# Optimization experiments

Measured on AMD Instinct MI355X. Metric: run time of the kernel, lower is better.

## Reference

```python
import jax, jax.numpy as jnp
import numpy as np
from jax import lax

NPOINT, RADIUS, NSAMPLE = 512, 0.2, 32
MLP, IN_CH = (64, 64, 128), 6
BN_EPS = 1e-5


def square_distance(src, dst):
    # src [B,S,3], dst [B,N,3] -> [B,S,N]
    d = -2.0 * jnp.einsum('bsc,bnc->bsn', src, dst)
    d += jnp.sum(src ** 2, -1)[:, :, None]
    d += jnp.sum(dst ** 2, -1)[:, None, :]
    return d


def farthest_point_sample(xyz, npoint):
    # deterministic start at index 0 (torch version uses randint)
    B, N, _ = xyz.shape
    init_dist = jnp.full((B, N), 1e10, dtype=xyz.dtype)
    init_far = jnp.zeros((B,), dtype=jnp.int32)

    def step(carry, _):
        distance, farthest = carry
        centroid = jnp.take_along_axis(xyz, farthest[:, None, None], axis=1)  # [B,1,3]
        dist = jnp.sum((xyz - centroid) ** 2, -1)  # [B,N]
        distance = jnp.minimum(distance, dist)
        nxt = jnp.argmax(distance, -1).astype(jnp.int32)
        return (distance, nxt), farthest

    _, cents = lax.scan(step, (init_dist, init_far), None, length=npoint)
    return cents.T  # [B, npoint]


def index_points(points, idx):
    # points [B,N,C], idx [B,...] -> [B,...,C]
    return jax.vmap(lambda p, i: p[i])(points, idx)


def query_ball_point(radius, nsample, xyz, new_xyz):
    B, N, _ = xyz.shape
    sqr = square_distance(new_xyz, xyz)  # [B,S,N]
    gi = jnp.where(sqr > radius ** 2, N, jnp.arange(N, dtype=jnp.int32)[None, None, :])
    gi = jnp.sort(gi, axis=-1)[:, :, :nsample]  # [B,S,K]
    first = gi[:, :, :1]
    return jnp.where(gi == N, first, gi)


def setup_inputs():
    key = jax.random.key(0)
    ks = jax.random.split(key, 2 + len(MLP))
    B, N = 16, 4096
    inp = {
        'xyz': jax.random.normal(ks[0], (B, N, 3), dtype=jnp.float32),
        'points': jax.random.normal(ks[1], (B, N, 3), dtype=jnp.float32),
    }
    last = IN_CH
    for i, oc in enumerate(MLP):
        inp[f'w{i}'] = jax.random.normal(ks[2 + i], (oc, last), dtype=jnp.float32) / np.sqrt(last)
        inp[f'b{i}'] = jnp.zeros((oc,), dtype=jnp.float32)
        inp[f'gamma{i}'] = jnp.ones((oc,), dtype=jnp.float32)
        inp[f'beta{i}'] = jnp.zeros((oc,), dtype=jnp.float32)
        last = oc
    return inp


def reference(xyz, points, w0, b0, gamma0, beta0, w1, b1, gamma1, beta1, w2, b2, gamma2, beta2):
    B, N, C = xyz.shape
    S = NPOINT
    fps_idx = lax.stop_gradient(farthest_point_sample(xyz, NPOINT))  # [B,S]
    new_xyz = index_points(xyz, fps_idx)  # [B,S,3]
    idx = lax.stop_gradient(query_ball_point(RADIUS, NSAMPLE, xyz, new_xyz))  # [B,S,K]
    grouped_xyz = index_points(xyz, idx)  # [B,S,K,3]
    grouped_xyz_norm = grouped_xyz - new_xyz[:, :, None, :]
    grouped_points = index_points(points, idx)  # [B,S,K,D]
    feats = jnp.concatenate([grouped_xyz_norm, grouped_points], axis=-1)  # [B,S,K,3+D]

    # shared MLP: 1x1 conv + BatchNorm (batch stats, train-mode) + ReLU, channel-last
    params = [(w0, b0, gamma0, beta0), (w1, b1, gamma1, beta1), (w2, b2, gamma2, beta2)]
    for w, b, g, be in params:
        feats = jnp.einsum('bskc,oc->bsko', feats, w) + b
        mean = jnp.mean(feats, axis=(0, 1, 2))
        var = jnp.var(feats, axis=(0, 1, 2))
        feats = (feats - mean) * lax.rsqrt(var + BN_EPS) * g + be
        feats = jax.nn.relu(feats)

    new_points = jnp.max(feats, axis=2)  # max over nsample -> [B,S,C_out]
    return new_xyz, new_points
```

## Files before the change

### kernel.cpp

```cpp
#include <hip/hip_runtime.h>

#define NPT    4096
#define NBATCH 16
#define NS     512
#define KSAMP  32
#define MROWS  (NBATCH*NS*KSAMP)
#define RC2    0.04f
#define NZSTAT 3288

using bf16x8 = __attribute__((ext_vector_type(8))) short;
using f32x4  = __attribute__((ext_vector_type(4))) float;
using f32x2  = __attribute__((ext_vector_type(2))) float;
#define MFMA16(A,B,C) __builtin_amdgcn_mfma_f32_16x16x32_bf16(A,B,C,0,0,0)

__device__ __forceinline__ unsigned short f2bf(float f) {
  unsigned u = __float_as_uint(f);
  unsigned r = (u + 0x7FFFu + ((u >> 16) & 1u)) >> 16;
  return (unsigned short)r;
}
__device__ __forceinline__ float bf2f(unsigned short h) {
  return __uint_as_float(((unsigned)h) << 16);
}
__device__ __forceinline__ void atomAddF64(double* p, double v) {
  unsafeAtomicAdd(p, v);
}

template<int CTRL>
__device__ __forceinline__ double dpp_max(double v) {
  long long x = __double_as_longlong(v);
  int lo = __builtin_amdgcn_update_dpp(0, (int)(x & 0xFFFFFFFFll), CTRL, 0xf, 0xf, true);
  int hi = __builtin_amdgcn_update_dpp(0, (int)(x >> 32),          CTRL, 0xf, 0xf, true);
  return fmax(v, __hiloint2double(hi, lo));
}

__global__ __launch_bounds__(512) void fps_wconv_kernel(const float* __restrict__ xyz,
                                                        float* __restrict__ out_newxyz,
                                                        float* __restrict__ ws_newxyz,
                                                        const float* __restrict__ w0,
                                                        const float* __restrict__ w1,
                                                        const float* __restrict__ w2,
                                                        unsigned short* __restrict__ wbf0,
                                                        unsigned short* __restrict__ wbf1,
                                                        unsigned short* __restrict__ wbf2,
                                                        double* __restrict__ statz)
{
  const int t = threadIdx.x;
  const int b = blockIdx.x;
  if (b == NBATCH) {
    if (t < 64) {
#pragma unroll
      for (int c = 0; c < 8; ++c)
        wbf0[t*8 + c] = (c < 6) ? f2bf(w0[t*6 + c]) : (unsigned short)0;
    }
    for (int i = t; i < 64*64; i += 512) wbf1[i] = f2bf(w1[i]);
    for (int i = t; i < 128*64; i += 512) wbf2[i] = f2bf(w2[i]);
    for (int i = t; i < NZSTAT; i += 512) statz[i] = 0.0;
    return;
  }

  __shared__ float pts[NPT*3];
  __shared__ float cent[NS*3];
  __shared__ double red[8];
  __shared__ int farslot;
  const float* xb = xyz + (size_t)b * NPT * 3;

  { const float4* s4 = (const float4*)xb;
    float4* d4 = (float4*)pts;
    for (int i = t; i < NPT*3/4; i += 512) d4[i] = s4[i]; }
  __syncthreads();

  f32x2 px[4], py[4], pz[4], dist[4];
  unsigned int loc0[4], loc1[4];
#pragma unroll
  for (int j = 0; j < 4; ++j) {
    int i0 = t + (2*j)   * 512;
    int i1 = t + (2*j+1) * 512;
    px[j] = f32x2{pts[i0*3+0], pts[i1*3+0]};
    py[j] = f32x2{pts[i0*3+1], pts[i1*3+1]};
    pz[j] = f32x2{pts[i0*3+2], pts[i1*3+2]};
    dist[j] = f32x2{1e10f, 1e10f};
    loc0[j] = ~(unsigned)i0;
    loc1[j] = ~(unsigned)i1;
  }

  const int lane = t & 63, w = t >> 6;
  int far = 0;
  for (int s = 0; s < NS; ++s) {
    const float cx = pts[far*3+0], cy = pts[far*3+1], cz = pts[far*3+2];
    if (t == 0) { cent[s*3+0] = cx; cent[s*3+1] = cy; cent[s*3+2] = cz; }
    if (s == NS-1) break;

    double best = 0.0;
    {
#pragma clang fp contract(off)
      const f32x2 vcx = {cx, cx}, vcy = {cy, cy}, vcz = {cz, cz};
#pragma unroll
      for (int j = 0; j < 4; ++j) {
        f32x2 dx = px[j] - vcx;
        f32x2 dy = py[j] - vcy;
        f32x2 dz = pz[j] - vcz;
        f32x2 dd = dx*dx + dy*dy + dz*dz;
        f32x2 nd;
        nd.x = fminf(dist[j].x, dd.x);
        nd.y = fminf(dist[j].y, dd.y);
        dist[j] = nd;
        unsigned long long k0 = ((unsigned long long)__float_as_uint(nd.x) << 32)
                              | (unsigned long long)loc0[j];
        unsigned long long k1 = ((unsigned long long)__float_as_uint(nd.y) << 32)
                              | (unsigned long long)loc1[j];
        best = fmax(best, __longlong_as_double((long long)k0));
        best = fmax(best, __longlong_as_double((long long)k1));
      }
    }
    best = dpp_max<0x111>(best);
    best = dpp_max<0x112>(best);
    best = dpp_max<0x114>(best);
    best = dpp_max<0x118>(best);
    best = dpp_max<0x142>(best);
    best = dpp_max<0x143>(best);

    if (lane == 63) red[w] = best;
    __syncthreads();
    if (w == 0) {
      double v = red[lane & 7];
      v = dpp_max<0x111>(v);
      v = dpp_max<0x112>(v);
      v = dpp_max<0x114>(v);
      if (lane == 7)
        farslot = (int)(~(unsigned)(unsigned long long)__double_as_longlong(v));
    }
    __syncthreads();
    far = farslot;
  }
  __syncthreads();
  for (int i = t; i < NS*3; i += 512) {
    float v = cent[i];
    out_newxyz[(size_t)b*NS*3 + i] = v;
    ws_newxyz[(size_t)b*NS*3 + i]  = v;
  }
}

__global__ __launch_bounds__(256) void ball_kernel(const float* __restrict__ xyz,
                                                   const float* __restrict__ pointsf,
                                                   const float* __restrict__ ws_newxyz,
                                                   unsigned short* __restrict__ featsbf,
                                                   double* __restrict__ momb)
{
  __shared__ int sel[4][KSAMP];
  __shared__ float momw[4][27];
  const int t = threadIdx.x, lane = t & 63, w = t >> 6;
  const int q = blockIdx.x * 4 + w;
  const int b = q >> 9;
  const float* xb = xyz     + (size_t)b * NPT * 3;
  const float* pb = pointsf + (size_t)b * NPT * 3;

  const float qx = ws_newxyz[q*3+0], qy = ws_newxyz[q*3+1], qz = ws_newxyz[q*3+2];
  const float q2 = __fadd_rn(__fadd_rn(__fmul_rn(qx,qx), __fmul_rn(qy,qy)), __fmul_rn(qz,qz));

  int count = 0;
  for (int c = 0; c < 64 && count < KSAMP; ++c) {
    int i = (c << 6) + lane;
    float fx = xb[i*3+0], fy = xb[i*3+1], fz = xb[i*3+2];
    float p2 = __fadd_rn(__fadd_rn(__fmul_rn(fx,fx), __fmul_rn(fy,fy)), __fmul_rn(fz,fz));
    float e  = __fadd_rn(__fadd_rn(__fmul_rn(qx,fx), __fmul_rn(qy,fy)), __fmul_rn(qz,fz));
    float d  = __fadd_rn(__fadd_rn(__fmul_rn(-2.0f, e), q2), p2);
    bool keep = (d <= RC2);
    unsigned long long mask = __ballot(keep ? 1 : 0);
    int slot = count + (int)__popcll(mask & ((1ull << lane) - 1ull));
    if (keep && slot < KSAMP) sel[w][slot] = i;
    count += (int)__popcll(mask);
  }
  __syncthreads();

  float f[6];
  const int n = (count < KSAMP) ? count : KSAMP;
  if (lane < KSAMP) {
    int id = (lane < n) ? sel[w][lane] : sel[w][0];
    float gx = xb[id*3+0], gy = xb[id*3+1], gz = xb[id*3+2];
    unsigned short hb[8];
    hb[0] = f2bf(__fsub_rn(gx, qx));
    hb[1] = f2bf(__fsub_rn(gy, qy));
    hb[2] = f2bf(__fsub_rn(gz, qz));
    hb[3] = f2bf(pb[id*3+0]);
    hb[4] = f2bf(pb[id*3+1]);
    hb[5] = f2bf(pb[id*3+2]);
    hb[6] = 0; hb[7] = 0;
    uint4 pk;
    pk.x = (unsigned)hb[0] | ((unsigned)hb[1] << 16);
    pk.y = (unsigned)hb[2] | ((unsigned)hb[3] << 16);
    pk.z = (unsigned)hb[4] | ((unsigned)hb[5] << 16);
    pk.w = 0;
    ((uint4*)featsbf)[(size_t)q * KSAMP + lane] = pk;
#pragma unroll
    for (int c2 = 0; c2 < 6; ++c2) f[c2] = bf2f(hb[c2]);
  } else {
    f[0]=f[1]=f[2]=f[3]=f[4]=f[5]=0.f;
  }

  float p[27];
#pragma unroll
  for (int c = 0; c < 6; ++c) p[c] = f[c];
  { int m = 6;
#pragma unroll
    for (int c = 0; c < 6; ++c)
#pragma unroll
      for (int d = c; d < 6; ++d) p[m++] = f[c]*f[d]; }
#pragma unroll
  for (int mm = 0; mm < 27; ++mm) {
    float v = p[mm];
#pragma unroll
    for (int off = 1; off < 64; off <<= 1) v += __shfl_xor(v, off);
    p[mm] = v;
  }
  if (lane == 0) {
#pragma unroll
    for (int mm = 0; mm < 27; ++mm) momw[w][mm] = p[mm];
  }
  __syncthreads();
  if (t < 27)
    atomAddF64(&momb[(blockIdx.x & 7)*27 + t],
               (double)(momw[0][t] + momw[1][t] + momw[2][t] + momw[3][t]));
}

template<int PASS>
__global__ __launch_bounds__(256) void mlp_kernel(
    const unsigned short* __restrict__ featsbf,
    const unsigned short* __restrict__ wbf0,
    const unsigned short* __restrict__ wbf1,
    const unsigned short* __restrict__ wbf2,
    const double* __restrict__ momb,
    const float* __restrict__ g0, const float* __restrict__ be0,
    const float* __restrict__ g1, const float* __restrict__ be1,
    const float* __restrict__ g2, const float* __restrict__ be2,
    double* __restrict__ s1g, double* __restrict__ q1g,
    double* __restrict__ s2g, double* __restrict__ q2g,
    float* __restrict__ outp)
{
  __shared__ __align__(16) unsigned short xb[256*72];
  __shared__ __align__(16) unsigned short wb[128*72];
  constexpr int SN = (PASS==1) ? 4*64 : (PASS==2 ? 4*128 : 1);
  __shared__ float ssum[SN], sqsum[SN];
  __shared__ float ssc0[64], ssh0[64], ssc1[64], ssh1[64], ssc2[128], ssh2[128];
  __shared__ double mom[27];

  unsigned short* wb0 = wb + 64*72;
  unsigned short* xf  = wb + 72*72;

  const int t = threadIdx.x, blk = blockIdx.x;
  const int lane = t & 63, w = t >> 6;
  const int lr = lane & 15, lk = lane >> 4;

  ((uint4*)xf)[t] = ((const uint4*)featsbf)[(size_t)blk*256 + t];
  if (t < 64) ((uint4*)wb0)[t] = ((const uint4*)wbf0)[t];
  { int row = t >> 2, seg = t & 3;
    const uint4* src = (const uint4*)(wbf1 + row*64 + seg*16);
    uint4* dst = (uint4*)(wb + row*72 + seg*16);
    dst[0] = src[0]; dst[1] = src[1]; }
  if (t < 27) {
    double s = 0.0;
#pragma unroll
    for (int bkt = 0; bkt < 8; ++bkt) s += momb[bkt*27 + t];
    mom[t] = s / (double)MROWS;
  }
  __syncthreads();

  if (t < 64) {
    double wv[6];
#pragma unroll
    for (int c = 0; c < 6; ++c) wv[c] = (double)bf2f(wbf0[t*8 + c]);
    double macc = 0.0;
#pragma unroll
    for (int c = 0; c < 6; ++c) macc += wv[c] * mom[c];
    double e2 = 0.0;
    int mi = 6;
#pragma unroll
    for (int c = 0; c < 6; ++c)
#pragma unroll
      for (int d = c; d < 6; ++d) {
        double coef = (c == d) ? wv[c]*wv[c] : 2.0*wv[c]*wv[d];
        e2 += coef * mom[mi++];
      }
    double var = e2 - macc*macc;
    float sc = g0[t] / sqrtf((float)var + 1e-5f);
    ssc0[t] = sc;
    ssh0[t] = be0[t] - (float)macc * sc;
  }
  if (PASS >= 2 && t < 64) {
    double s = 0.0, qq = 0.0;
#pragma unroll
    for (int bkt = 0; bkt < 8; ++bkt) { s += s1g[bkt*64 + t]; qq += q1g[bkt*64 + t]; }
    double mean = s / (double)MROWS;
    double var  = qq / (double)MROWS - mean*mean;
    float sc = g1[t] / sqrtf((float)var + 1e-5f);
    ssc1[t] = sc;
    ssh1[t] = be1[t] - (float)mean * sc;
  }
  if (PASS == 3 && t < 128) {
    double s = 0.0, qq = 0.0;
#pragma unroll
    for (int bkt = 0; bkt < 8; ++bkt) { s += s2g[bkt*128 + t]; qq += q2g[bkt*128 + t]; }
    double mean = s / (double)MROWS;
    double var  = qq / (double)MROWS - mean*mean;
    float sc = g2[t] / sqrtf((float)var + 1e-5f);
    ssc2[t] = sc;
    ssh2[t] = be2[t] - (float)mean * sc;
  }
  __syncthreads();

  const bf16x8 zb = {0,0,0,0,0,0,0,0};
  const f32x4 fz = {0.f,0.f,0.f,0.f};

  f32x4 acc[16];
#pragma unroll
  for (int i = 0; i < 16; ++i) acc[i] = fz;
  {
    bf16x8 af[4], bw[4];
#pragma unroll
    for (int i = 0; i < 4; ++i) { af[i] = zb; bw[i] = zb; }
    if (lk == 0) {
#pragma unroll
      for (int rt = 0; rt < 4; ++rt) af[rt] = *(const bf16x8*)&xf[(w*64 + rt*16 + lr)*8];
#pragma unroll
      for (int ct = 0; ct < 4; ++ct) bw[ct] = *(const bf16x8*)&wb0[(ct*16 + lr)*8];
    }
#pragma unroll
    for (int rt = 0; rt < 4; ++rt)
#pragma unroll
      for (int ct = 0; ct < 4; ++ct) acc[rt*4+ct] = MFMA16(af[rt], bw[ct], acc[rt*4+ct]);
  }
#pragma unroll
  for (int rt = 0; rt < 4; ++rt)
#pragma unroll
    for (int ct = 0; ct < 4; ++ct) {
      const int ch = ct*16 + lr;
      const float sc = ssc0[ch], sh = ssh0[ch];
#pragma unroll
      for (int r = 0; r < 4; ++r) {
        const int row = w*64 + rt*16 + lk*4 + r;
        float v = fmaxf(fmaf(acc[rt*4+ct][r], sc, sh), 0.f);
        xb[row*72 + ch] = f2bf(v);
      }
    }
  __syncthreads();

  f32x4 acc1[16];
#pragma unroll
  for (int i = 0; i < 16; ++i) acc1[i] = fz;
#pragma unroll
  for (int k0 = 0; k0 < 64; k0 += 32) {
    bf16x8 af[4], bw[4];
#pragma unroll
    for (int rt = 0; rt < 4; ++rt) af[rt] = *(const bf16x8*)&xb[(w*64 + rt*16 + lr)*72 + k0 + lk*8];
#pragma unroll
    for (int ct = 0; ct < 4; ++ct) bw[ct] = *(const bf16x8*)&wb[(ct*16 + lr)*72 + k0 + lk*8];
#pragma unroll
    for (int rt = 0; rt < 4; ++rt)
#pragma unroll
      for (int ct = 0; ct < 4; ++ct) acc1[rt*4+ct] = MFMA16(af[rt], bw[ct], acc1[rt*4+ct]);
  }

  if (PASS == 1) {
#pragma unroll
    for (int ct = 0; ct < 4; ++ct) {
      float s = 0.f, q = 0.f;
#pragma unroll
      for (int rt = 0; rt < 4; ++rt)
#pragma unroll
        for (int r = 0; r < 4; ++r) { float v = acc1[rt*4+ct][r]; s += v; q = fmaf(v, v, q); }
      s += __shfl_xor(s, 16); s += __shfl_xor(s, 32);
      q += __shfl_xor(q, 16); q += __shfl_xor(q, 32);
      if (lk == 0) { ssum[w*64 + ct*16 + lr] = s; sqsum[w*64 + ct*16 + lr] = q; }
    }
    __syncthreads();
    if (t < 64) {
      float s = ssum[t] + ssum[64+t] + ssum[128+t] + ssum[192+t];
      float q = sqsum[t] + sqsum[64+t] + sqsum[128+t] + sqsum[192+t];
      const int bkt = blk & 7;
      atomAddF64(&s1g[bkt*64 + t], (double)s);
      atomAddF64(&q1g[bkt*64 + t], (double)q);
    }
    return;
  }

  __syncthreads();

  { int row = t >> 1, seg = t & 1;
    const uint4* src = (const uint4*)(wbf2 + row*64 + seg*32);
    uint4* dst = (uint4*)(wb + row*72 + seg*32);
    dst[0] = src[0]; dst[1] = src[1]; dst[2] = src[2]; dst[3] = src[3]; }
#pragma unroll
  for (int rt = 0; rt < 4; ++rt)
#pragma unroll
    for (int ct = 0; ct < 4; ++ct) {
      const int ch = ct*16 + lr;
      const float sc = ssc1[ch], sh = ssh1[ch];
#pragma unroll
      for (int r = 0; r < 4; ++r) {
        const int row = w*64 + rt*16 + lk*4 + r;
        float v = fmaxf(fmaf(acc1[rt*4+ct][r], sc, sh), 0.f);
        xb[row*72 + ch] = f2bf(v);
      }
    }
  __syncthreads();

#pragma unroll
  for (int half = 0; half < 2; ++half) {
    f32x4 acc2[16];
#pragma unroll
    for (int i = 0; i < 16; ++i) acc2[i] = fz;
#pragma unroll
    for (int k0 = 0; k0 < 64; k0 += 32) {
      bf16x8 af[4], bw[4];
#pragma unroll
      for (int rt = 0; rt < 4; ++rt) af[rt] = *(const bf16x8*)&xb[(w*64 + rt*16 + lr)*72 + k0 + lk*8];
#pragma unroll
      for (int ct = 0; ct < 4; ++ct) bw[ct] = *(const bf16x8*)&wb[((half*4+ct)*16 + lr)*72 + k0 + lk*8];
#pragma unroll
      for (int rt = 0; rt < 4; ++rt)
#pragma unroll
        for (int ct = 0; ct < 4; ++ct) acc2[rt*4+ct] = MFMA16(af[rt], bw[ct], acc2[rt*4+ct]);
    }
    if (PASS == 2) {
#pragma unroll
      for (int ct = 0; ct < 4; ++ct) {
        float s = 0.f, q = 0.f;
#pragma unroll
        for (int rt = 0; rt < 4; ++rt)
#pragma unroll
          for (int r = 0; r < 4; ++r) { float v = acc2[rt*4+ct][r]; s += v; q = fmaf(v, v, q); }
        s += __shfl_xor(s, 16); s += __shfl_xor(s, 32);
        q += __shfl_xor(q, 16); q += __shfl_xor(q, 32);
        const int ch = (half*4+ct)*16 + lr;
        if (lk == 0) { ssum[w*128 + ch] = s; sqsum[w*128 + ch] = q; }
      }
    } else {
#pragma unroll
      for (int ct = 0; ct < 4; ++ct) {
        const int ch = (half*4+ct)*16 + lr;
        const float sc = ssc2[ch], sh = ssh2[ch];
        float ma = 0.f, mb = 0.f;
#pragma unroll
        for (int r = 0; r < 4; ++r) {
          ma = fmaxf(ma, fmaf(acc2[0*4+ct][r], sc, sh));
          ma = fmaxf(ma, fmaf(acc2[1*4+ct][r], sc, sh));
          mb = fmaxf(mb, fmaf(acc2[2*4+ct][r], sc, sh));
          mb = fmaxf(mb, fmaf(acc2[3*4+ct][r], sc, sh));
        }
        ma = fmaxf(ma, __shfl_xor(ma, 16)); ma = fmaxf(ma, __shfl_xor(ma, 32));
        mb = fmaxf(mb, __shfl_xor(mb, 16)); mb = fmaxf(mb, __shfl_xor(mb, 32));
        if (lk == 0) {
          const int q0 = blk*8 + w*2;
          outp[(size_t)q0*128 + ch]     = ma;
          outp[(size_t)(q0+1)*128 + ch] = mb;
        }
      }
    }
  }
  if (PASS == 2) {
    __syncthreads();
    if (t < 128) {
      float s = ssum[t] + ssum[128+t] + ssum[256+t] + ssum[384+t];
      float q = sqsum[t] + sqsum[128+t] + sqsum[256+t] + sqsum[384+t];
      const int bkt = blk & 7;
      atomAddF64(&s2g[bkt*128 + t], (double)s);
      atomAddF64(&q2g[bkt*128 + t], (double)q);
    }
  }
}

extern "C" void kernel_launch(void* const* d_in, const int* in_sizes, int n_in,
                              void* d_out, int out_size, void* d_ws, size_t ws_size,
                              hipStream_t stream)
{
  const float* xyz     = (const float*)d_in[0];
  const float* pointsf = (const float*)d_in[1];
  const float* w0  = (const float*)d_in[2];
  const float* g0  = (const float*)d_in[4];
  const float* be0 = (const float*)d_in[5];
  const float* w1  = (const float*)d_in[6];
  const float* g1  = (const float*)d_in[8];
  const float* be1 = (const float*)d_in[9];
  const float* w2  = (const float*)d_in[10];
  const float* g2  = (const float*)d_in[12];
  const float* be2 = (const float*)d_in[13];

  float* out        = (float*)d_out;
  float* out_newxyz = out;
  float* out_newpts = out + 24576;

  float* ws = (float*)d_ws;
  float* ws_newxyz = ws;
  unsigned short* featsbf = (unsigned short*)(ws + 24576);
  double* momb = (double*)(ws + 1073152);
  double* s1g  = momb + 216;
  double* q1g  = s1g + 512;
  double* s2g  = q1g + 512;
  double* q2g  = s2g + 1024;
  unsigned short* wbf0 = (unsigned short*)(ws + 1079728);
  unsigned short* wbf1 = (unsigned short*)(ws + 1079984);
  unsigned short* wbf2 = (unsigned short*)(ws + 1082032);

  fps_wconv_kernel<<<NBATCH + 1, 512, 0, stream>>>(xyz, out_newxyz, ws_newxyz,
      w0, w1, w2, wbf0, wbf1, wbf2, momb);
  ball_kernel<<<2048, 256, 0, stream>>>(xyz, pointsf, ws_newxyz, featsbf, momb);
  mlp_kernel<1><<<1024, 256, 0, stream>>>(featsbf, wbf0, wbf1, wbf2, momb,
      g0, be0, g1, be1, g2, be2, s1g, q1g, s2g, q2g, nullptr);
  mlp_kernel<2><<<1024, 256, 0, stream>>>(featsbf, wbf0, wbf1, wbf2, momb,
      g0, be0, g1, be1, g2, be2, s1g, q1g, s2g, q2g, nullptr);
  mlp_kernel<3><<<1024, 256, 0, stream>>>(featsbf, wbf0, wbf1, wbf2, momb,
      g0, be0, g1, be1, g2, be2, s1g, q1g, s2g, q2g, out_newpts);
}
```

Measured before the change: 446.9 us.

## Fuse ball query and three MLP passes into one cooperative kernel with grid syncs

Merges the ball-query kernel and the three MLP stat/output passes into a single cooperative mega-kernel of 512 persistent blocks, separated by grid-wide syncs. Each block loops over several tiles and computes BN scale/shift only once per pass. This is meant to remove the launch gaps and tail effects between four kernels. The FPS reduction also drops its second block barrier by double-buffering the per-wave maxima so every thread reduces them directly. Risks: grid.sync cost, lower occupancy from the combined shared memory, and a fallback to the old multi-kernel path if the cooperative launch fails.

```diff
diff --git a/kernel.cpp b/kernel.cpp
--- a/kernel.cpp
+++ b/kernel.cpp
@@ -1,4 +1,6 @@
 #include <hip/hip_runtime.h>
+#include <hip/hip_cooperative_groups.h>
+namespace cg = cooperative_groups;
 
 #define NPT    4096
 #define NBATCH 16
@@ -60,8 +62,7 @@
 
   __shared__ float pts[NPT*3];
   __shared__ float cent[NS*3];
-  __shared__ double red[8];
-  __shared__ int farslot;
+  __shared__ __align__(16) double red[2][8];
   const float* xb = xyz + (size_t)b * NPT * 3;
 
   { const float4* s4 = (const float4*)xb;
@@ -119,18 +120,14 @@
     best = dpp_max<0x142>(best);
     best = dpp_max<0x143>(best);
 
-    if (lane == 63) red[w] = best;
+    if (lane == 63) red[s & 1][w] = best;
     __syncthreads();
-    if (w == 0) {
-      double v = red[lane & 7];
-      v = dpp_max<0x111>(v);
-      v = dpp_max<0x112>(v);
-      v = dpp_max<0x114>(v);
-      if (lane == 7)
-        farslot = (int)(~(unsigned)(unsigned long long)__double_as_longlong(v));
-    }
-    __syncthreads();
-    far = farslot;
+    { const double2* r2 = (const double2*)red[s & 1];
+      double2 a = r2[0], b2 = r2[1], c = r2[2], d = r2[3];
+      double m = fmax(fmax(fmax(a.x, a.y), fmax(b2.x, b2.y)),
+                      fmax(fmax(c.x, c.y), fmax(d.x, d.y)));
+      far = (int)(~(unsigned)(unsigned long long)__double_as_longlong(m));
+    }
   }
   __syncthreads();
   for (int i = t; i < NS*3; i += 512) {
@@ -140,16 +137,27 @@
   }
 }
 
-__global__ __launch_bounds__(256) void ball_kernel(const float* __restrict__ xyz,
-                                                   const float* __restrict__ pointsf,
-                                                   const float* __restrict__ ws_newxyz,
-                                                   unsigned short* __restrict__ featsbf,
-                                                   double* __restrict__ momb)
-{
-  __shared__ int sel[4][KSAMP];
-  __shared__ float momw[4][27];
+struct __align__(16) MlpSmem {
+  unsigned short xb[256*72];
+  unsigned short wb[128*72];
+  float ssum[512], sqsum[512];
+  float ssc0[64], ssh0[64], ssc1[64], ssh1[64], ssc2[128], ssh2[128];
+  double mom[27];
+};
+struct BallSmem {
+  int sel[4][KSAMP];
+  float momw[4][27];
+};
+
+__device__ __forceinline__ void ball_tile(int tile, BallSmem& bs,
+                                          const float* __restrict__ xyz,
+                                          const float* __restrict__ pointsf,
+                                          const float* __restrict__ ws_newxyz,
+                                          unsigned short* __restrict__ featsbf,
+                                          double* __restrict__ momb)
+{
   const int t = threadIdx.x, lane = t & 63, w = t >> 6;
-  const int q = blockIdx.x * 4 + w;
+  const int q = tile * 4 + w;
   const int b = q >> 9;
   const float* xb = xyz     + (size_t)b * NPT * 3;
   const float* pb = pointsf + (size_t)b * NPT * 3;
@@ -167,7 +175,7 @@
     bool keep = (d <= RC2);
     unsigned long long mask = __ballot(keep ? 1 : 0);
     int slot = count + (int)__popcll(mask & ((1ull << lane) - 1ull));
-    if (keep && slot < KSAMP) sel[w][slot] = i;
+    if (keep && slot < KSAMP) bs.sel[w][slot] = i;
     count += (int)__popcll(mask);
   }
   __syncthreads();
@@ -175,7 +183,7 @@
   float f[6];
   const int n = (count < KSAMP) ? count : KSAMP;
   if (lane < KSAMP) {
-    int id = (lane < n) ? sel[w][lane] : sel[w][0];
+    int id = (lane < n) ? bs.sel[w][lane] : bs.sel[w][0];
     float gx = xb[id*3+0], gy = xb[id*3+1], gz = xb[id*3+2];
     unsigned short hb[8];
     hb[0] = f2bf(__fsub_rn(gx, qx));
@@ -184,7 +192,6 @@
     hb[3] = f2bf(pb[id*3+0]);
     hb[4] = f2bf(pb[id*3+1]);
     hb[5] = f2bf(pb[id*3+2]);
-    hb[6] = 0; hb[7] = 0;
     uint4 pk;
     pk.x = (unsigned)hb[0] | ((unsigned)hb[1] << 16);
     pk.y = (unsigned)hb[2] | ((unsigned)hb[3] << 16);
@@ -214,12 +221,304 @@
   }
   if (lane == 0) {
 #pragma unroll
-    for (int mm = 0; mm < 27; ++mm) momw[w][mm] = p[mm];
+    for (int mm = 0; mm < 27; ++mm) bs.momw[w][mm] = p[mm];
   }
   __syncthreads();
   if (t < 27)
-    atomAddF64(&momb[(blockIdx.x & 7)*27 + t],
-               (double)(momw[0][t] + momw[1][t] + momw[2][t] + momw[3][t]));
+    atomAddF64(&momb[(tile & 7)*27 + t],
+               (double)(bs.momw[0][t] + bs.momw[1][t] + bs.momw[2][t] + bs.momw[3][t]));
+  __syncthreads();
+}
+
+template<int PASS>
+__device__ __forceinline__ void mlp_tile(int tile, int prolog, MlpSmem& sm,
+    const unsigned short* __restrict__ featsbf,
+    const unsigned short* __restrict__ wbf0,
+    const unsigned short* __restrict__ wbf1,
+    const unsigned short* __restrict__ wbf2,
+    const double* __restrict__ momb,
+    const float* __restrict__ g0, const float* __restrict__ be0,
+    const float* __restrict__ g1, const float* __restrict__ be1,
+    const float* __restrict__ g2, const float* __restrict__ be2,
+    double* __restrict__ s1g, double* __restrict__ q1g,
+    double* __restrict__ s2g, double* __restrict__ q2g,
+    float* __restrict__ outp)
+{
+  unsigned short* wb0 = sm.wb + 64*72;
+  unsigned short* xf  = sm.wb + 72*72;
+
+  const int t = threadIdx.x;
+  const int lane = t & 63, w = t >> 6;
+  const int lr = lane & 15, lk = lane >> 4;
+
+  ((uint4*)xf)[t] = ((const uint4*)featsbf)[(size_t)tile*256 + t];
+  if (t < 64) ((uint4*)wb0)[t] = ((const uint4*)wbf0)[t];
+  { int row = t >> 2, seg = t & 3;
+    const uint4* src = (const uint4*)(wbf1 + row*64 + seg*16);
+    uint4* dst = (uint4*)(sm.wb + row*72 + seg*16);
+    dst[0] = src[0]; dst[1] = src[1]; }
+  if ((prolog & 1) && t < 27) {
+    double s = 0.0;
+#pragma unroll
+    for (int bkt = 0; bkt < 8; ++bkt) s += momb[bkt*27 + t];
+    sm.mom[t] = s / (double)MROWS;
+  }
+  __syncthreads();
+
+  if ((prolog & 1) && t < 64) {
+    double wv[6];
+#pragma unroll
+    for (int c = 0; c < 6; ++c) wv[c] = (double)bf2f(wbf0[t*8 + c]);
+    double macc = 0.0;
+#pragma unroll
+    for (int c = 0; c < 6; ++c) macc += wv[c] * sm.mom[c];
+    double e2 = 0.0;
+    int mi = 6;
+#pragma unroll
+    for (int c = 0; c < 6; ++c)
+#pragma unroll
+      for (int d = c; d < 6; ++d) {
+        double coef = (c == d) ? wv[c]*wv[c] : 2.0*wv[c]*wv[d];
+        e2 += coef * sm.mom[mi++];
+      }
+    double var = e2 - macc*macc;
+    float sc = g0[t] / sqrtf((float)var + 1e-5f);
+    sm.ssc0[t] = sc;
+    sm.ssh0[t] = be0[t] - (float)macc * sc;
+  }
+  if ((prolog & 2) && t < 64) {
+    double s = 0.0, qq = 0.0;
+#pragma unroll
+    for (int bkt = 0; bkt < 8; ++bkt) { s += s1g[bkt*64 + t]; qq += q1g[bkt*64 + t]; }
+    double mean = s / (double)MROWS;
+    double var  = qq / (double)MROWS - mean*mean;
+    float sc = g1[t] / sqrtf((float)var + 1e-5f);
+    sm.ssc1[t] = sc;
+    sm.ssh1[t] = be1[t] - (float)mean * sc;
+  }
+  if ((prolog & 4) && t < 128) {
+    double s = 0.0, qq = 0.0;
+#pragma unroll
+    for (int bkt = 0; bkt < 8; ++bkt) { s += s2g[bkt*128 + t]; qq += q2g[bkt*128 + t]; }
+    double mean = s / (double)MROWS;
+    double var  = qq / (double)MROWS - mean*mean;
+    float sc = g2[t] / sqrtf((float)var + 1e-5f);
+    sm.ssc2[t] = sc;
+    sm.ssh2[t] = be2[t] - (float)mean * sc;
+  }
+  __syncthreads();
+
+  const bf16x8 zb = {0,0,0,0,0,0,0,0};
+  const f32x4 fz = {0.f,0.f,0.f,0.f};
+
+  f32x4 acc[16];
+#pragma unroll
+  for (int i = 0; i < 16; ++i) acc[i] = fz;
+  {
+    bf16x8 af[4], bw[4];
+#pragma unroll
+    for (int i = 0; i < 4; ++i) { af[i] = zb; bw[i] = zb; }
+    if (lk == 0) {
+#pragma unroll
+      for (int rt = 0; rt < 4; ++rt) af[rt] = *(const bf16x8*)&xf[(w*64 + rt*16 + lr)*8];
+#pragma unroll
+      for (int ct = 0; ct < 4; ++ct) bw[ct] = *(const bf16x8*)&wb0[(ct*16 + lr)*8];
+    }
+#pragma unroll
+    for (int rt = 0; rt < 4; ++rt)
+#pragma unroll
+      for (int ct = 0; ct < 4; ++ct) acc[rt*4+ct] = MFMA16(af[rt], bw[ct], acc[rt*4+ct]);
+  }
+#pragma unroll
+  for (int rt = 0; rt < 4; ++rt)
+#pragma unroll
+    for (int ct = 0; ct < 4; ++ct) {
+      const int ch = ct*16 + lr;
+      const float sc = sm.ssc0[ch], sh = sm.ssh0[ch];
+#pragma unroll
+      for (int r = 0; r < 4; ++r) {
+        const int row = w*64 + rt*16 + lk*4 + r;
+        float v = fmaxf(fmaf(acc[rt*4+ct][r], sc, sh), 0.f);
+        sm.xb[row*72 + ch] = f2bf(v);
+      }
+    }
+  __syncthreads();
+
+  f32x4 acc1[16];
+#pragma unroll
+  for (int i = 0; i < 16; ++i) acc1[i] = fz;
+#pragma unroll
+  for (int k0 = 0; k0 < 64; k0 += 32) {
+    bf16x8 af[4], bw[4];
+#pragma unroll
+    for (int rt = 0; rt < 4; ++rt) af[rt] = *(const bf16x8*)&sm.xb[(w*64 + rt*16 + lr)*72 + k0 + lk*8];
+#pragma unroll
+    for (int ct = 0; ct < 4; ++ct) bw[ct] = *(const bf16x8*)&sm.wb[(ct*16 + lr)*72 + k0 + lk*8];
+#pragma unroll
+    for (int rt = 0; rt < 4; ++rt)
+#pragma unroll
+      for (int ct = 0; ct < 4; ++ct) acc1[rt*4+ct] = MFMA16(af[rt], bw[ct], acc1[rt*4+ct]);
+  }
+
+  if constexpr (PASS == 1) {
+#pragma unroll
+    for (int ct = 0; ct < 4; ++ct) {
+      float s = 0.f, q = 0.f;
+#pragma unroll
+      for (int rt = 0; rt < 4; ++rt)
+#pragma unroll
+        for (int r = 0; r < 4; ++r) { float v = acc1[rt*4+ct][r]; s += v; q = fmaf(v, v, q); }
+      s += __shfl_xor(s, 16); s += __shfl_xor(s, 32);
+      q += __shfl_xor(q, 16); q += __shfl_xor(q, 32);
+      if (lk == 0) { sm.ssum[w*64 + ct*16 + lr] = s; sm.sqsum[w*64 + ct*16 + lr] = q; }
+    }
+    __syncthreads();
+    if (t < 64) {
+      float s = sm.ssum[t] + sm.ssum[64+t] + sm.ssum[128+t] + sm.ssum[192+t];
+      float q = sm.sqsum[t] + sm.sqsum[64+t] + sm.sqsum[128+t] + sm.sqsum[192+t];
+      const int bkt = tile & 7;
+      atomAddF64(&s1g[bkt*64 + t], (double)s);
+      atomAddF64(&q1g[bkt*64 + t], (double)q);
+    }
+    __syncthreads();
+    return;
+  }
+
+  __syncthreads();
+
+  { int row = t >> 1, seg = t & 1;
+    const uint4* src = (const uint4*)(wbf2 + row*64 + seg*32);
+    uint4* dst = (uint4*)(sm.wb + row*72 + seg*32);
+    dst[0] = src[0]; dst[1] = src[1]; dst[2] = src[2]; dst[3] = src[3]; }
+#pragma unroll
+  for (int rt = 0; rt < 4; ++rt)
+#pragma unroll
+    for (int ct = 0; ct < 4; ++ct) {
+      const int ch = ct*16 + lr;
+      const float sc = sm.ssc1[ch], sh = sm.ssh1[ch];
+#pragma unroll
+      for (int r = 0; r < 4; ++r) {
+        const int row = w*64 + rt*16 + lk*4 + r;
+        float v = fmaxf(fmaf(acc1[rt*4+ct][r], sc, sh), 0.f);
+        sm.xb[row*72 + ch] = f2bf(v);
+      }
+    }
+  __syncthreads();
+
+#pragma unroll
+  for (int half = 0; half < 2; ++half) {
+    f32x4 acc2[16];
+#pragma unroll
+    for (int i = 0; i < 16; ++i) acc2[i] = fz;
+#pragma unroll
+    for (int k0 = 0; k0 < 64; k0 += 32) {
+      bf16x8 af[4], bw[4];
+#pragma unroll
+      for (int rt = 0; rt < 4; ++rt) af[rt] = *(const bf16x8*)&sm.xb[(w*64 + rt*16 + lr)*72 + k0 + lk*8];
+#pragma unroll
+      for (int ct = 0; ct < 4; ++ct) bw[ct] = *(const bf16x8*)&sm.wb[((half*4+ct)*16 + lr)*72 + k0 + lk*8];
+#pragma unroll
+      for (int rt = 0; rt < 4; ++rt)
+#pragma unroll
+        for (int ct = 0; ct < 4; ++ct) acc2[rt*4+ct] = MFMA16(af[rt], bw[ct], acc2[rt*4+ct]);
+    }
+    if constexpr (PASS == 2) {
+#pragma unroll
+      for (int ct = 0; ct < 4; ++ct) {
+        float s = 0.f, q = 0.f;
+#pragma unroll
+        for (int rt = 0; rt < 4; ++rt)
+#pragma unroll
+          for (int r = 0; r < 4; ++r) { float v = acc2[rt*4+ct][r]; s += v; q = fmaf(v, v, q); }
+        s += __shfl_xor(s, 16); s += __shfl_xor(s, 32);
+        q += __shfl_xor(q, 16); q += __shfl_xor(q, 32);
+        const int ch = (half*4+ct)*16 + lr;
+        if (lk == 0) { sm.ssum[w*128 + ch] = s; sm.sqsum[w*128 + ch] = q; }
+      }
+    } else {
+#pragma unroll
+      for (int ct = 0; ct < 4; ++ct) {
+        const int ch = (half*4+ct)*16 + lr;
+        const float sc = sm.ssc2[ch], sh = sm.ssh2[ch];
+        float ma = 0.f, mb = 0.f;
+#pragma unroll
+        for (int r = 0; r < 4; ++r) {
+          ma = fmaxf(ma, fmaf(acc2[0*4+ct][r], sc, sh));
+          ma = fmaxf(ma, fmaf(acc2[1*4+ct][r], sc, sh));
+          mb = fmaxf(mb, fmaf(acc2[2*4+ct][r], sc, sh));
+          mb = fmaxf(mb, fmaf(acc2[3*4+ct][r], sc, sh));
+        }
+        ma = fmaxf(ma, __shfl_xor(ma, 16)); ma = fmaxf(ma, __shfl_xor(ma, 32));
+        mb = fmaxf(mb, __shfl_xor(mb, 16)); mb = fmaxf(mb, __shfl_xor(mb, 32));
+        if (lk == 0) {
+          const int q0 = tile*8 + w*2;
+          outp[(size_t)q0*128 + ch]     = ma;
+          outp[(size_t)(q0+1)*128 + ch] = mb;
+        }
+      }
+    }
+  }
+  if constexpr (PASS == 2) {
+    __syncthreads();
+    if (t < 128) {
+      float s = sm.ssum[t] + sm.ssum[128+t] + sm.ssum[256+t] + sm.ssum[384+t];
+      float q = sm.sqsum[t] + sm.sqsum[128+t] + sm.sqsum[256+t] + sm.sqsum[384+t];
+      const int bkt = tile & 7;
+      atomAddF64(&s2g[bkt*128 + t], (double)s);
+      atomAddF64(&q2g[bkt*128 + t], (double)q);
+    }
+  }
+  __syncthreads();
+}
+
+#define MLP_ARGS featsbf, wbf0, wbf1, wbf2, momb, g0, be0, g1, be1, g2, be2, \
+                 s1g, q1g, s2g, q2g, outp
+
+__global__ __launch_bounds__(256, 2) void mega_kernel(
+    const float* __restrict__ xyz, const float* __restrict__ pointsf,
+    const float* __restrict__ ws_newxyz,
+    unsigned short* __restrict__ featsbf, double* __restrict__ momb,
+    const unsigned short* __restrict__ wbf0,
+    const unsigned short* __restrict__ wbf1,
+    const unsigned short* __restrict__ wbf2,
+    const float* __restrict__ g0, const float* __restrict__ be0,
+    const float* __restrict__ g1, const float* __restrict__ be1,
+    const float* __restrict__ g2, const float* __restrict__ be2,
+    double* __restrict__ s1g, double* __restrict__ q1g,
+    double* __restrict__ s2g, double* __restrict__ q2g,
+    float* __restrict__ outp)
+{
+  __shared__ MlpSmem sm;
+  __shared__ BallSmem bs;
+  cg::grid_group grid = cg::this_grid();
+  const int blk = blockIdx.x;
+
+#pragma unroll 1
+  for (int i = 0; i < 4; ++i)
+    ball_tile(blk*4 + i, bs, xyz, pointsf, ws_newxyz, featsbf, momb);
+  __threadfence();
+  grid.sync();
+#pragma unroll 1
+  for (int i = 0; i < 2; ++i)
+    mlp_tile<1>(blk*2 + i, (i == 0) ? 1 : 0, sm, MLP_ARGS);
+  __threadfence();
+  grid.sync();
+#pragma unroll 1
+  for (int i = 0; i < 2; ++i)
+    mlp_tile<2>(blk*2 + i, (i == 0) ? 2 : 0, sm, MLP_ARGS);
+  __threadfence();
+  grid.sync();
+#pragma unroll 1
+  for (int i = 0; i < 2; ++i)
+    mlp_tile<3>(blk*2 + i, (i == 0) ? 4 : 0, sm, MLP_ARGS);
+}
+
+__global__ __launch_bounds__(256) void ball_kernel(const float* __restrict__ xyz,
+    const float* __restrict__ pointsf, const float* __restrict__ ws_newxyz,
+    unsigned short* __restrict__ featsbf, double* __restrict__ momb)
+{
+  __shared__ BallSmem bs;
+  ball_tile(blockIdx.x, bs, xyz, pointsf, ws_newxyz, featsbf, momb);
 }
 
 template<int PASS>
@@ -236,236 +535,9 @@
     double* __restrict__ s2g, double* __restrict__ q2g,
     float* __restrict__ outp)
 {
-  __shared__ __align__(16) unsigned short xb[256*72];
-  __shared__ __align__(16) unsigned short wb[128*72];
-  constexpr int SN = (PASS==1) ? 4*64 : (PASS==2 ? 4*128 : 1);
-  __shared__ float ssum[SN], sqsum[SN];
-  __shared__ float ssc0[64], ssh0[64], ssc1[64], ssh1[64], ssc2[128], ssh2[128];
-  __shared__ double mom[27];
-
-  unsigned short* wb0 = wb + 64*72;
-  unsigned short* xf  = wb + 72*72;
-
-  const int t = threadIdx.x, blk = blockIdx.x;
-  const int lane = t & 63, w = t >> 6;
-  const int lr = lane & 15, lk = lane >> 4;
-
-  ((uint4*)xf)[t] = ((const uint4*)featsbf)[(size_t)blk*256 + t];
-  if (t < 64) ((uint4*)wb0)[t] = ((const uint4*)wbf0)[t];
-  { int row = t >> 2, seg = t & 3;
-    const uint4* src = (const uint4*)(wbf1 + row*64 + seg*16);
-    uint4* dst = (uint4*)(wb + row*72 + seg*16);
-    dst[0] = src[0]; dst[1] = src[1]; }
-  if (t < 27) {
-    double s = 0.0;
-#pragma unroll
-    for (int bkt = 0; bkt < 8; ++bkt) s += momb[bkt*27 + t];
-    mom[t] = s / (double)MROWS;
-  }
-  __syncthreads();
-
-  if (t < 64) {
-    double wv[6];
-#pragma unroll
-    for (int c = 0; c < 6; ++c) wv[c] = (double)bf2f(wbf0[t*8 + c]);
-    double macc = 0.0;
-#pragma unroll
-    for (int c = 0; c < 6; ++c) macc += wv[c] * mom[c];
-    double e2 = 0.0;
-    int mi = 6;
-#pragma unroll
-    for (int c = 0; c < 6; ++c)
-#pragma unroll
-      for (int d = c; d < 6; ++d) {
-        double coef = (c == d) ? wv[c]*wv[c] : 2.0*wv[c]*wv[d];
-        e2 += coef * mom[mi++];
-      }
-    double var = e2 - macc*macc;
-    float sc = g0[t] / sqrtf((float)var + 1e-5f);
-    ssc0[t] = sc;
-    ssh0[t] = be0[t] - (float)macc * sc;
-  }
-  if (PASS >= 2 && t < 64) {
-    double s = 0.0, qq = 0.0;
-#pragma unroll
-    for (int bkt = 0; bkt < 8; ++bkt) { s += s1g[bkt*64 + t]; qq += q1g[bkt*64 + t]; }
-    double mean = s / (double)MROWS;
-    double var  = qq / (double)MROWS - mean*mean;
-    float sc = g1[t] / sqrtf((float)var + 1e-5f);
-    ssc1[t] = sc;
-    ssh1[t] = be1[t] - (float)mean * sc;
-  }
-  if (PASS == 3 && t < 128) {
-    double s = 0.0, qq = 0.0;
-#pragma unroll
-    for (int bkt = 0; bkt < 8; ++bkt) { s += s2g[bkt*128 + t]; qq += q2g[bkt*128 + t]; }
-    double mean = s / (double)MROWS;
-    double var  = qq / (double)MROWS - mean*mean;
-    float sc = g2[t] / sqrtf((float)var + 1e-5f);
-    ssc2[t] = sc;
-    ssh2[t] = be2[t] - (float)mean * sc;
-  }
-  __syncthreads();
-
-  const bf16x8 zb = {0,0,0,0,0,0,0,0};
-  const f32x4 fz = {0.f,0.f,0.f,0.f};
-
-  f32x4 acc[16];
-#pragma unroll
-  for (int i = 0; i < 16; ++i) acc[i] = fz;
-  {
-    bf16x8 af[4], bw[4];
-#pragma unroll
-    for (int i = 0; i < 4; ++i) { af[i] = zb; bw[i] = zb; }
-    if (lk == 0) {
-#pragma unroll
-      for (int rt = 0; rt < 4; ++rt) af[rt] = *(const bf16x8*)&xf[(w*64 + rt*16 + lr)*8];
-#pragma unroll
-      for (int ct = 0; ct < 4; ++ct) bw[ct] = *(const bf16x8*)&wb0[(ct*16 + lr)*8];
-    }
-#pragma unroll
-    for (int rt = 0; rt < 4; ++rt)
-#pragma unroll
-      for (int ct = 0; ct < 4; ++ct) acc[rt*4+ct] = MFMA16(af[rt], bw[ct], acc[rt*4+ct]);
-  }
-#pragma unroll
-  for (int rt = 0; rt < 4; ++rt)
-#pragma unroll
-    for (int ct = 0; ct < 4; ++ct) {
-      const int ch = ct*16 + lr;
-      const float sc = ssc0[ch], sh = ssh0[ch];
-#pragma unroll
-      for (int r = 0; r < 4; ++r) {
-        const int row = w*64 + rt*16 + lk*4 + r;
-        float v = fmaxf(fmaf(acc[rt*4+ct][r], sc, sh), 0.f);
-        xb[row*72 + ch] = f2bf(v);
-      }
-    }
-  __syncthreads();
-
-  f32x4 acc1[16];
-#pragma unroll
-  for (int i = 0; i < 16; ++i) acc1[i] = fz;
-#pragma unroll
-  for (int k0 = 0; k0 < 64; k0 += 32) {
-    bf16x8 af[4], bw[4];
-#pragma unroll
-    for (int rt = 0; rt < 4; ++rt) af[rt] = *(const bf16x8*)&xb[(w*64 + rt*16 + lr)*72 + k0 + lk*8];
-#pragma unroll
-    for (int ct = 0; ct < 4; ++ct) bw[ct] = *(const bf16x8*)&wb[(ct*16 + lr)*72 + k0 + lk*8];
-#pragma unroll
-    for (int rt = 0; rt < 4; ++rt)
-#pragma unroll
-      for (int ct = 0; ct < 4; ++ct) acc1[rt*4+ct] = MFMA16(af[rt], bw[ct], acc1[rt*4+ct]);
-  }
-
-  if (PASS == 1) {
-#pragma unroll
-    for (int ct = 0; ct < 4; ++ct) {
-      float s = 0.f, q = 0.f;
-#pragma unroll
-      for (int rt = 0; rt < 4; ++rt)
-#pragma unroll
-        for (int r = 0; r < 4; ++r) { float v = acc1[rt*4+ct][r]; s += v; q = fmaf(v, v, q); }
-      s += __shfl_xor(s, 16); s += __shfl_xor(s, 32);
-      q += __shfl_xor(q, 16); q += __shfl_xor(q, 32);
-      if (lk == 0) { ssum[w*64 + ct*16 + lr] = s; sqsum[w*64 + ct*16 + lr] = q; }
-    }
-    __syncthreads();
-    if (t < 64) {
-      float s = ssum[t] + ssum[64+t] + ssum[128+t] + ssum[192+t];
-      float q = sqsum[t] + sqsum[64+t] + sqsum[128+t] + sqsum[192+t];
-      const int bkt = blk & 7;
-      atomAddF64(&s1g[bkt*64 + t], (double)s);
-      atomAddF64(&q1g[bkt*64 + t], (double)q);
-    }
-    return;
-  }
-
-  __syncthreads();
-
-  { int row = t >> 1, seg = t & 1;
-    const uint4* src = (const uint4*)(wbf2 + row*64 + seg*32);
-    uint4* dst = (uint4*)(wb + row*72 + seg*32);
-    dst[0] = src[0]; dst[1] = src[1]; dst[2] = src[2]; dst[3] = src[3]; }
-#pragma unroll
-  for (int rt = 0; rt < 4; ++rt)
-#pragma unroll
-    for (int ct = 0; ct < 4; ++ct) {
-      const int ch = ct*16 + lr;
-      const float sc = ssc1[ch], sh = ssh1[ch];
-#pragma unroll
-      for (int r = 0; r < 4; ++r) {
-        const int row = w*64 + rt*16 + lk*4 + r;
-        float v = fmaxf(fmaf(acc1[rt*4+ct][r], sc, sh), 0.f);
-        xb[row*72 + ch] = f2bf(v);
-      }
-    }
-  __syncthreads();
-
-#pragma unroll
-  for (int half = 0; half < 2; ++half) {
-    f32x4 acc2[16];
-#pragma unroll
-    for (int i = 0; i < 16; ++i) acc2[i] = fz;
-#pragma unroll
-    for (int k0 = 0; k0 < 64; k0 += 32) {
-      bf16x8 af[4], bw[4];
-#pragma unroll
-      for (int rt = 0; rt < 4; ++rt) af[rt] = *(const bf16x8*)&xb[(w*64 + rt*16 + lr)*72 + k0 + lk*8];
-#pragma unroll
-      for (int ct = 0; ct < 4; ++ct) bw[ct] = *(const bf16x8*)&wb[((half*4+ct)*16 + lr)*72 + k0 + lk*8];
-#pragma unroll
-      for (int rt = 0; rt < 4; ++rt)
-#pragma unroll
-        for (int ct = 0; ct < 4; ++ct) acc2[rt*4+ct] = MFMA16(af[rt], bw[ct], acc2[rt*4+ct]);
-    }
-    if (PASS == 2) {
-#pragma unroll
-      for (int ct = 0; ct < 4; ++ct) {
-        float s = 0.f, q = 0.f;
-#pragma unroll
-        for (int rt = 0; rt < 4; ++rt)
-#pragma unroll
-          for (int r = 0; r < 4; ++r) { float v = acc2[rt*4+ct][r]; s += v; q = fmaf(v, v, q); }
-        s += __shfl_xor(s, 16); s += __shfl_xor(s, 32);
-        q += __shfl_xor(q, 16); q += __shfl_xor(q, 32);
-        const int ch = (half*4+ct)*16 + lr;
-        if (lk == 0) { ssum[w*128 + ch] = s; sqsum[w*128 + ch] = q; }
-      }
-    } else {
-#pragma unroll
-      for (int ct = 0; ct < 4; ++ct) {
-        const int ch = (half*4+ct)*16 + lr;
-        const float sc = ssc2[ch], sh = ssh2[ch];
-        float ma = 0.f, mb = 0.f;
-#pragma unroll
-        for (int r = 0; r < 4; ++r) {
-          ma = fmaxf(ma, fmaf(acc2[0*4+ct][r], sc, sh));
-          ma = fmaxf(ma, fmaf(acc2[1*4+ct][r], sc, sh));
-          mb = fmaxf(mb, fmaf(acc2[2*4+ct][r], sc, sh));
-          mb = fmaxf(mb, fmaf(acc2[3*4+ct][r], sc, sh));
-        }
-        ma = fmaxf(ma, __shfl_xor(ma, 16)); ma = fmaxf(ma, __shfl_xor(ma, 32));
-        mb = fmaxf(mb, __shfl_xor(mb, 16)); mb = fmaxf(mb, __shfl_xor(mb, 32));
-        if (lk == 0) {
-          const int q0 = blk*8 + w*2;
-          outp[(size_t)q0*128 + ch]     = ma;
-          outp[(size_t)(q0+1)*128 + ch] = mb;
-        }
-      }
-    }
-  }
-  if (PASS == 2) {
-    __syncthreads();
-    if (t < 128) {
-      float s = ssum[t] + ssum[128+t] + ssum[256+t] + ssum[384+t];
-      float q = sqsum[t] + sqsum[128+t] + sqsum[256+t] + sqsum[384+t];
-      const int bkt = blk & 7;
-      atomAddF64(&s2g[bkt*128 + t], (double)s);
-      atomAddF64(&q2g[bkt*128 + t], (double)q);
-    }
-  }
+  __shared__ MlpSmem sm;
+  constexpr int prolog = (PASS == 1) ? 1 : (PASS == 2 ? 3 : 7);
+  mlp_tile<PASS>(blockIdx.x, prolog, sm, MLP_ARGS);
 }
 
 extern "C" void kernel_launch(void* const* d_in, const int* in_sizes, int n_in,
@@ -502,11 +574,24 @@
 
   fps_wconv_kernel<<<NBATCH + 1, 512, 0, stream>>>(xyz, out_newxyz, ws_newxyz,
       w0, w1, w2, wbf0, wbf1, wbf2, momb);
-  ball_kernel<<<2048, 256, 0, stream>>>(xyz, pointsf, ws_newxyz, featsbf, momb);
-  mlp_kernel<1><<<1024, 256, 0, stream>>>(featsbf, wbf0, wbf1, wbf2, momb,
-      g0, be0, g1, be1, g2, be2, s1g, q1g, s2g, q2g, nullptr);
-  mlp_kernel<2><<<1024, 256, 0, stream>>>(featsbf, wbf0, wbf1, wbf2, momb,
-      g0, be0, g1, be1, g2, be2, s1g, q1g, s2g, q2g, nullptr);
-  mlp_kernel<3><<<1024, 256, 0, stream>>>(featsbf, wbf0, wbf1, wbf2, momb,
-      g0, be0, g1, be1, g2, be2, s1g, q1g, s2g, q2g, out_newpts);
-}
+
+  void* kargs[] = { (void*)&xyz, (void*)&pointsf, (void*)&ws_newxyz,
+                    (void*)&featsbf, (void*)&momb,
+                    (void*)&wbf0, (void*)&wbf1, (void*)&wbf2,
+                    (void*)&g0, (void*)&be0, (void*)&g1, (void*)&be1,
+                    (void*)&g2, (void*)&be2,
+                    (void*)&s1g, (void*)&q1g, (void*)&s2g, (void*)&q2g,
+                    (void*)&out_newpts };
+  hipError_t err = hipLaunchCooperativeKernel((void*)mega_kernel,
+                                              dim3(512), dim3(256),
+                                              kargs, 0, stream);
+  if (err != hipSuccess) {
+    ball_kernel<<<2048, 256, 0, stream>>>(xyz, pointsf, ws_newxyz, featsbf, momb);
+    mlp_kernel<1><<<1024, 256, 0, stream>>>(featsbf, wbf0, wbf1, wbf2, momb,
+        g0, be0, g1, be1, g2, be2, s1g, q1g, s2g, q2g, nullptr);
+    mlp_kernel<2><<<1024, 256, 0, stream>>>(featsbf, wbf0, wbf1, wbf2, momb,
+        g0, be0, g1, be1, g2, be2, s1g, q1g, s2g, q2g, nullptr);
+    mlp_kernel<3><<<1024, 256, 0, stream>>>(featsbf, wbf0, wbf1, wbf2, momb,
+        g0, be0, g1, be1, g2, be2, s1g, q1g, s2g, q2g, out_newpts);
+  }
+}
```

New measurement: 753.5 us. +68.6%, slower.
